# Kernel tuning notes

Measured on AMD Instinct MI355X. Metric: run time of the kernel, lower is better.

## Reference

```python
import jax, jax.numpy as jnp
import numpy as np

N_NODES = 100000
N_EDGES = 1600000
D_IN = 128
D_H = 128
N_CLASSES = 64


def setup_inputs() -> dict:
    key = jax.random.key(0)
    ks = jax.random.split(key, 8)
    feat = jax.random.normal(ks[0], (N_NODES, D_IN), dtype=jnp.float32)
    src = jax.random.randint(ks[1], (N_EDGES,), 0, N_NODES)
    dst = jax.random.randint(ks[2], (N_EDGES,), 0, N_NODES)
    # Xavier-ish scaled weights (nn.Linear layout: [out, in])
    W1 = jax.random.normal(ks[3], (D_H, D_IN), dtype=jnp.float32) * (1.0 / np.sqrt(D_IN))
    b1 = jnp.zeros((D_H,), dtype=jnp.float32)
    W2 = jax.random.normal(ks[4], (D_H, D_H), dtype=jnp.float32) * (1.0 / np.sqrt(D_H))
    b2 = jnp.zeros((D_H,), dtype=jnp.float32)
    Wl = jax.random.normal(ks[5], (N_CLASSES, 2 * D_H), dtype=jnp.float32) * (1.0 / np.sqrt(2 * D_H))
    bl = jnp.zeros((N_CLASSES,), dtype=jnp.float32)
    return {"feat": feat, "src": src, "dst": dst, "W1": W1, "b1": b1,
            "W2": W2, "b2": b2, "Wl": Wl, "bl": bl}


def _mean_agg(h, src, dst, inv_deg, n):
    # copy_u('h','m') + mean('m','neigh'): gather src features, segment-sum on dst, divide by in-degree
    s = jax.ops.segment_sum(h[src], dst, num_segments=n)  # [N, D]
    return s * inv_deg


def reference(feat, src, dst, W1, b1, W2, b2, Wl, bl):
    n = feat.shape[0]
    deg = jax.ops.segment_sum(jnp.ones_like(dst, dtype=feat.dtype), dst, num_segments=n)
    inv_deg = (1.0 / jnp.maximum(deg, 1.0))[:, None]  # zero-degree nodes -> 0 (sum is 0 anyway)
    h1 = jax.nn.relu(_mean_agg(feat, src, dst, inv_deg, n) @ W1.T + b1)
    h2 = jax.nn.relu(_mean_agg(h1, src, dst, inv_deg, n) @ W2.T + b2)
    logits = jnp.concatenate([h1, h2], axis=-1) @ Wl.T + bl
    return jax.nn.log_softmax(logits, axis=-1)
```

## Files before the change

### kernel.cpp

```cpp
#include <hip/hip_runtime.h>
#include <stdint.h>

#define D 128
#define NCLS 64
#define BSH 7
#define NBMAX 1024
#define CCHUNK 4096

typedef __bf16 bf16x8 __attribute__((ext_vector_type(8)));
typedef float f32x4 __attribute__((ext_vector_type(4)));
typedef float f32x2 __attribute__((ext_vector_type(2)));

union B8 { uint4 u; bf16x8 v; };


__global__ __launch_bounds__(256) void k_prep(const float* __restrict__ feat,
                                              const float* __restrict__ W1,
                                              const float* __restrict__ W2,
                                              const float* __restrict__ Wl,
                                              ushort* __restrict__ featb,
                                              ushort* __restrict__ W1b,
                                              ushort* __restrict__ W2b,
                                              ushort* __restrict__ Wlb,
                                              int* __restrict__ bcnt, int n8feat) {
  const int n1 = D * D / 8;
  const int nl = 2 * D * NCLS / 8;
  int t = blockIdx.x * 256 + threadIdx.x;
  if (t < NBMAX) bcnt[t] = 0;
  const float* xp; ushort* yp; int idx;
  if (t < n8feat) { xp = feat; yp = featb; idx = t; }
  else {
    t -= n8feat;
    if (t < n1) { xp = W1; yp = W1b; idx = t; }
    else if (t < 2 * n1) { xp = W2; yp = W2b; idx = t - n1; }
    else if (t < 2 * n1 + nl) { xp = Wl; yp = Wlb; idx = t - 2 * n1; }
    else return;
  }
  const float4 a = reinterpret_cast<const float4*>(xp)[idx * 2 + 0];
  const float4 b = reinterpret_cast<const float4*>(xp)[idx * 2 + 1];
  union { __bf16 h[8]; uint4 u; } p;
  p.h[0] = (__bf16)a.x; p.h[1] = (__bf16)a.y; p.h[2] = (__bf16)a.z; p.h[3] = (__bf16)a.w;
  p.h[4] = (__bf16)b.x; p.h[5] = (__bf16)b.y; p.h[6] = (__bf16)b.z; p.h[7] = (__bf16)b.w;
  reinterpret_cast<uint4*>(yp)[idx] = p.u;
}


__global__ __launch_bounds__(256) void k_bhist(const int* __restrict__ dst,
                                               int* __restrict__ bcnt, int E, int NB) {
  __shared__ int h[NBMAX];
  for (int i = threadIdx.x; i < NB; i += 256) h[i] = 0;
  __syncthreads();
  for (int e = blockIdx.x * 256 + threadIdx.x; e < E; e += gridDim.x * 256)
    atomicAdd(&h[dst[e] >> BSH], 1);
  __syncthreads();
  for (int i = threadIdx.x; i < NB; i += 256) {
    int c = h[i];
    if (c) atomicAdd(&bcnt[i], c);
  }
}

__global__ __launch_bounds__(1024) void k_bscan(const int* __restrict__ bcnt,
                                                int* __restrict__ bbase,
                                                int* __restrict__ bcur, int NB, int E) {
  __shared__ int sm[NBMAX];
  const int tid = threadIdx.x;
  int v = (tid < NB) ? bcnt[tid] : 0;
  sm[tid] = v;
  __syncthreads();
  for (int off = 1; off < NBMAX; off <<= 1) {
    int t = (tid >= off) ? sm[tid - off] : 0;
    __syncthreads();
    sm[tid] += t;
    __syncthreads();
  }
  if (tid < NB) {
    bbase[tid] = sm[tid] - v;
    bcur[tid] = sm[tid] - v;
  }
  if (tid == 0) bbase[NB] = E;
}

__global__ __launch_bounds__(256) void k_bscatter(const int* __restrict__ src,
                                                  const int* __restrict__ dst,
                                                  int* __restrict__ bcur,
                                                  int* __restrict__ ebuck, int E, int NB) {
  __shared__ int h[NBMAX];
  __shared__ int base[NBMAX];
  const int beg = blockIdx.x * CCHUNK;
  const int end = min(beg + CCHUNK, E);
  for (int i = threadIdx.x; i < NB; i += 256) h[i] = 0;
  __syncthreads();
  for (int e = beg + threadIdx.x; e < end; e += 256)
    atomicAdd(&h[dst[e] >> BSH], 1);
  __syncthreads();
  for (int i = threadIdx.x; i < NB; i += 256) {
    int c = h[i];
    base[i] = c ? atomicAdd(&bcur[i], c) : 0;
    h[i] = 0;
  }
  __syncthreads();
  for (int e = beg + threadIdx.x; e < end; e += 256) {
    const int d = dst[e];
    const int b = d >> BSH;
    const int r = atomicAdd(&h[b], 1);
    ebuck[base[b] + r] = (src[e] << BSH) | (d & 127);
  }
}

__global__ __launch_bounds__(256) void k_bbuild(const int* __restrict__ ebuck,
                                                const int* __restrict__ bbase,
                                                int* __restrict__ row_ptr,
                                                int* __restrict__ esrc,
                                                float* __restrict__ inv, int N, int E) {
  __shared__ int cnt[128], s[128], cur[128];
  const int b = blockIdx.x;
  const int n0 = b << BSH;
  const int nn = min(128, N - n0);
  const int beg = bbase[b], end = bbase[b + 1];
  const int tid = threadIdx.x;
  if (tid < 128) cnt[tid] = 0;
  __syncthreads();
  for (int e = beg + tid; e < end; e += 256)
    atomicAdd(&cnt[ebuck[e] & 127], 1);
  __syncthreads();
  if (tid < 128) s[tid] = cnt[tid];
  __syncthreads();
  for (int off = 1; off < 128; off <<= 1) {
    int t = (tid < 128 && tid >= off) ? s[tid - off] : 0;
    __syncthreads();
    if (tid < 128) s[tid] += t;
    __syncthreads();
  }
  if (tid < 128) {
    const int ex = s[tid] - cnt[tid];
    cur[tid] = ex;
    if (tid < nn) {
      row_ptr[n0 + tid] = beg + ex;
      inv[n0 + tid] = 1.0f / fmaxf((float)cnt[tid], 1.0f);
    }
  }
  if (b == 0 && tid == 0) row_ptr[N] = E;
  __syncthreads();
  for (int e = beg + tid; e < end; e += 256) {
    const int p = ebuck[e];
    const int r = atomicAdd(&cur[p & 127], 1);
    esrc[beg + r] = p >> BSH;
  }
}


__device__ __forceinline__ void accp(f32x2& a, unsigned int u) {
  f32x2 v;
  v.x = __uint_as_float(u << 16);
  v.y = __uint_as_float(u & 0xffff0000u);
  a += v;
}

__device__ __forceinline__ void acc8p(f32x2 acc[4], const uint4& u) {
  accp(acc[0], u.x);
  accp(acc[1], u.y);
  accp(acc[2], u.z);
  accp(acc[3], u.w);
}

__device__ __forceinline__ void gather_tile(const ushort* __restrict__ h,
                                            const int* __restrict__ row_ptr,
                                            const int* __restrict__ esrc,
                                            const float* __restrict__ inv,
                                            ushort At[16][136],
                                            int mt, int nl, int l15, int N) {
  const int node = mt * 16 + nl;
  const ushort* hp = h + l15 * 8;
  f32x2 acc[4] = {{0.f, 0.f}, {0.f, 0.f}, {0.f, 0.f}, {0.f, 0.f}};
  float iv = 0.f;
  if (node < N) {
    const int beg = row_ptr[node];
    const int end = row_ptr[node + 1];
    iv = inv[node];
    int e = beg;
    for (; e + 3 < end; e += 4) {
      const int4 ss = *reinterpret_cast<const int4*>(esrc + e);
      const uint4 u0 = *reinterpret_cast<const uint4*>(hp + (size_t)ss.x * D);
      const uint4 u1 = *reinterpret_cast<const uint4*>(hp + (size_t)ss.y * D);
      const uint4 u2 = *reinterpret_cast<const uint4*>(hp + (size_t)ss.z * D);
      const uint4 u3 = *reinterpret_cast<const uint4*>(hp + (size_t)ss.w * D);
      acc8p(acc, u0);
      acc8p(acc, u1);
      acc8p(acc, u2);
      acc8p(acc, u3);
    }
    for (; e < end; ++e) {
      const int s0 = esrc[e];
      const uint4 u0 = *reinterpret_cast<const uint4*>(hp + (size_t)s0 * D);
      acc8p(acc, u0);
    }
  }
  union { __bf16 b[8]; uint4 u; } p;
#pragma unroll
  for (int i = 0; i < 4; ++i) {
    p.b[i * 2 + 0] = (__bf16)(acc[i].x * iv);
    p.b[i * 2 + 1] = (__bf16)(acc[i].y * iv);
  }
  *reinterpret_cast<uint4*>(&At[nl][l15 * 8]) = p.u;
}


__global__ __launch_bounds__(256, 6) void k_fused1(const ushort* __restrict__ h,
                                                   const int* __restrict__ row_ptr,
                                                   const int* __restrict__ esrc,
                                                   const float* __restrict__ inv,
                                                   const ushort* __restrict__ Wb,
                                                   const float* __restrict__ bias,
                                                   ushort* __restrict__ Hout, int N) {
  __shared__ ushort At[16][136];
  const int wave = threadIdx.x >> 6;
  const int lane = threadIdx.x & 63;
  const int l15 = lane & 15;
  const int quad = lane >> 4;
  const int nl = wave * 4 + quad;

  B8 bfrag[2][4];
  float bv[2];
#pragma unroll
  for (int t = 0; t < 2; ++t) {
    const int n = wave * 32 + t * 16 + l15;
    bv[t] = bias[n];
#pragma unroll
    for (int ks = 0; ks < 4; ++ks)
      bfrag[t][ks].u = *reinterpret_cast<const uint4*>(Wb + n * D + ks * 32 + quad * 8);
  }

  const int mtiles = (N + 15) >> 4;
  for (int mt = blockIdx.x; mt < mtiles; mt += gridDim.x) {
    gather_tile(h, row_ptr, esrc, inv, At, mt, nl, l15, N);
    __syncthreads();
    const ushort* ap = &At[l15][quad * 8];
    B8 a0, a1, a2, a3;
    a0.u = *reinterpret_cast<const uint4*>(ap);
    a1.u = *reinterpret_cast<const uint4*>(ap + 32);
    a2.u = *reinterpret_cast<const uint4*>(ap + 64);
    a3.u = *reinterpret_cast<const uint4*>(ap + 96);
#pragma unroll
    for (int t = 0; t < 2; ++t) {
      f32x4 acc = {0.f, 0.f, 0.f, 0.f};
      acc = __builtin_amdgcn_mfma_f32_16x16x32_bf16(a0.v, bfrag[t][0].v, acc, 0, 0, 0);
      acc = __builtin_amdgcn_mfma_f32_16x16x32_bf16(a1.v, bfrag[t][1].v, acc, 0, 0, 0);
      acc = __builtin_amdgcn_mfma_f32_16x16x32_bf16(a2.v, bfrag[t][2].v, acc, 0, 0, 0);
      acc = __builtin_amdgcn_mfma_f32_16x16x32_bf16(a3.v, bfrag[t][3].v, acc, 0, 0, 0);
      const int col = wave * 32 + t * 16 + l15;
#pragma unroll
      for (int r = 0; r < 4; ++r) {
        const int row = mt * 16 + quad * 4 + r;
        if (row < N) {
          const float v = fmaxf(acc[r] + bv[t], 0.f);
          union { __bf16 b; ushort s; } c;
          c.b = (__bf16)v;
          Hout[(size_t)row * D + col] = c.s;
        }
      }
    }
    __syncthreads();
  }
}


__global__ __launch_bounds__(256, 5) void k_fused2(const ushort* __restrict__ h,
                                                   const int* __restrict__ row_ptr,
                                                   const int* __restrict__ esrc,
                                                   const float* __restrict__ inv,
                                                   const ushort* __restrict__ W2b,
                                                   const float* __restrict__ b2,
                                                   const ushort* __restrict__ Wlb,
                                                   const float* __restrict__ bl,
                                                   float* __restrict__ out, int N) {
  __shared__ ushort At[16][136];
  __shared__ ushort H2t[16][136];
  __shared__ float L[16][NCLS + 4];
  const int wave = threadIdx.x >> 6;
  const int lane = threadIdx.x & 63;
  const int l15 = lane & 15;
  const int quad = lane >> 4;
  const int nl = wave * 4 + quad;

  B8 bfrag2[2][4];
  float bv2[2];
#pragma unroll
  for (int t = 0; t < 2; ++t) {
    const int n = wave * 32 + t * 16 + l15;
    bv2[t] = b2[n];
#pragma unroll
    for (int ks = 0; ks < 4; ++ks)
      bfrag2[t][ks].u = *reinterpret_cast<const uint4*>(W2b + n * D + ks * 32 + quad * 8);
  }
  B8 bfragL[8];
  const int nlc = wave * 16 + l15;
  const float bbl = bl[nlc];
#pragma unroll
  for (int ks = 0; ks < 8; ++ks)
    bfragL[ks].u = *reinterpret_cast<const uint4*>(Wlb + nlc * (2 * D) + ks * 32 + quad * 8);

  const int mtiles = (N + 15) >> 4;
  for (int mt = blockIdx.x; mt < mtiles; mt += gridDim.x) {
    gather_tile(h, row_ptr, esrc, inv, At, mt, nl, l15, N);
    __syncthreads();
    {
      const ushort* ap = &At[l15][quad * 8];
      B8 a0, a1, a2, a3;
      a0.u = *reinterpret_cast<const uint4*>(ap);
      a1.u = *reinterpret_cast<const uint4*>(ap + 32);
      a2.u = *reinterpret_cast<const uint4*>(ap + 64);
      a3.u = *reinterpret_cast<const uint4*>(ap + 96);
#pragma unroll
      for (int t = 0; t < 2; ++t) {
        f32x4 acc = {0.f, 0.f, 0.f, 0.f};
        acc = __builtin_amdgcn_mfma_f32_16x16x32_bf16(a0.v, bfrag2[t][0].v, acc, 0, 0, 0);
        acc = __builtin_amdgcn_mfma_f32_16x16x32_bf16(a1.v, bfrag2[t][1].v, acc, 0, 0, 0);
        acc = __builtin_amdgcn_mfma_f32_16x16x32_bf16(a2.v, bfrag2[t][2].v, acc, 0, 0, 0);
        acc = __builtin_amdgcn_mfma_f32_16x16x32_bf16(a3.v, bfrag2[t][3].v, acc, 0, 0, 0);
        const int col = wave * 32 + t * 16 + l15;
#pragma unroll
        for (int r = 0; r < 4; ++r) {
          const float v = fmaxf(acc[r] + bv2[t], 0.f);
          union { __bf16 b; ushort s; } c;
          c.b = (__bf16)v;
          H2t[quad * 4 + r][col] = c.s;
        }
      }
    }
    __syncthreads();
    {
      const int row = mt * 16 + l15;
      const int rowc = row < N ? row : N - 1;
      const size_t rb = (size_t)rowc * D + quad * 8;
      f32x4 acc = {0.f, 0.f, 0.f, 0.f};
      B8 a;
#pragma unroll
      for (int ks = 0; ks < 4; ++ks) {
        a.u = *reinterpret_cast<const uint4*>(h + rb + ks * 32);
        acc = __builtin_amdgcn_mfma_f32_16x16x32_bf16(a.v, bfragL[ks].v, acc, 0, 0, 0);
      }
#pragma unroll
      for (int ks = 0; ks < 4; ++ks) {
        a.u = *reinterpret_cast<const uint4*>(&H2t[l15][ks * 32 + quad * 8]);
        acc = __builtin_amdgcn_mfma_f32_16x16x32_bf16(a.v, bfragL[4 + ks].v, acc, 0, 0, 0);
      }
#pragma unroll
      for (int r = 0; r < 4; ++r)
        L[quad * 4 + r][wave * 16 + l15] = acc[r] + bbl;
    }
    __syncthreads();
#pragma unroll
    for (int r = 0; r < 4; ++r) {
      const int row = wave * 4 + r;
      float v = L[row][lane];
      float m = v;
#pragma unroll
      for (int off = 32; off > 0; off >>= 1) m = fmaxf(m, __shfl_xor(m, off));
      float e = __expf(v - m);
#pragma unroll
      for (int off = 32; off > 0; off >>= 1) e += __shfl_xor(e, off);
      const int orow = mt * 16 + row;
      if (orow < N) out[(size_t)orow * NCLS + lane] = v - m - __logf(e);
    }
    __syncthreads();
  }
}


extern "C" void kernel_launch(void* const* d_in, const int* in_sizes, int n_in,
                              void* d_out, int out_size, void* d_ws, size_t ws_size,
                              hipStream_t stream) {
  const float* feat = (const float*)d_in[0];
  const int* src = (const int*)d_in[1];
  const int* dst = (const int*)d_in[2];
  const float* W1 = (const float*)d_in[3];
  const float* b1 = (const float*)d_in[4];
  const float* W2 = (const float*)d_in[5];
  const float* b2 = (const float*)d_in[6];
  const float* Wl = (const float*)d_in[7];
  const float* bl = (const float*)d_in[8];
  float* out = (float*)d_out;

  const int N = in_sizes[0] / D;
  const int E = in_sizes[1];
  const int NB = (N + 127) >> BSH;

  float* ws = (float*)d_ws;
  float* inv = ws;
  ushort* featb = (ushort*)(inv + N);
  ushort* scratch = featb + (size_t)N * D;
  ushort* h1b = scratch + (size_t)N * D;
  int* row_ptr = (int*)(h1b + (size_t)N * D);
  int* esrc = row_ptr + N + 1;
  int* bcnt = esrc + E;
  int* bbase = bcnt + NBMAX;
  int* bcur = bbase + NBMAX + 1;
  ushort* W1b = (ushort*)(bcur + NBMAX);
  ushort* W2b = W1b + D * D;
  ushort* Wlb = W2b + D * D;
  int* ebuck = (int*)scratch;

  const int n8 = N * D / 8;
  const int prepTot = n8 + 2 * (D * D / 8) + (2 * D * NCLS / 8);
  k_prep<<<(prepTot + 255) / 256, 256, 0, stream>>>(feat, W1, W2, Wl,
                                                    featb, W1b, W2b, Wlb, bcnt, n8);

  k_bhist<<<256, 256, 0, stream>>>(dst, bcnt, E, NB);
  k_bscan<<<1, 1024, 0, stream>>>(bcnt, bbase, bcur, NB, E);
  k_bscatter<<<(E + CCHUNK - 1) / CCHUNK, 256, 0, stream>>>(src, dst, bcur, ebuck, E, NB);
  k_bbuild<<<NB, 256, 0, stream>>>(ebuck, bbase, row_ptr, esrc, inv, N, E);

  k_fused1<<<2048, 256, 0, stream>>>(featb, row_ptr, esrc, inv, W1b, b1, h1b, N);
  k_fused2<<<2048, 256, 0, stream>>>(h1b, row_ptr, esrc, inv, W2b, b2, Wlb, bl, out, N);
}
```

Before: 391.2 us.

## Transform features before mean aggregation and drop separate bf16 prep pass

Uses linearity to apply W1 and W2 per node before the neighbor mean, so the gather kernels only sum, add bias and apply ReLU, and the dense GEMMs run as separate streaming kernels. Weights and features are converted to bf16 inside the GEMM kernels, which removes the standalone prep kernel, and the histogram counters are zeroed with a memset. The intent is a cheaper gather/GEMM split and no extra full-feature conversion pass. In exchange it adds extra launches and writes and rereads the z1/z2 intermediates, and the ebuck scratch now aliases z2.

```diff
diff --git a/kernel.cpp b/kernel.cpp
--- a/kernel.cpp
+++ b/kernel.cpp
@@ -13,35 +13,11 @@
 
 union B8 { uint4 u; bf16x8 v; };
 
-
-__global__ __launch_bounds__(256) void k_prep(const float* __restrict__ feat,
-                                              const float* __restrict__ W1,
-                                              const float* __restrict__ W2,
-                                              const float* __restrict__ Wl,
-                                              ushort* __restrict__ featb,
-                                              ushort* __restrict__ W1b,
-                                              ushort* __restrict__ W2b,
-                                              ushort* __restrict__ Wlb,
-                                              int* __restrict__ bcnt, int n8feat) {
-  const int n1 = D * D / 8;
-  const int nl = 2 * D * NCLS / 8;
-  int t = blockIdx.x * 256 + threadIdx.x;
-  if (t < NBMAX) bcnt[t] = 0;
-  const float* xp; ushort* yp; int idx;
-  if (t < n8feat) { xp = feat; yp = featb; idx = t; }
-  else {
-    t -= n8feat;
-    if (t < n1) { xp = W1; yp = W1b; idx = t; }
-    else if (t < 2 * n1) { xp = W2; yp = W2b; idx = t - n1; }
-    else if (t < 2 * n1 + nl) { xp = Wl; yp = Wlb; idx = t - 2 * n1; }
-    else return;
-  }
-  const float4 a = reinterpret_cast<const float4*>(xp)[idx * 2 + 0];
-  const float4 b = reinterpret_cast<const float4*>(xp)[idx * 2 + 1];
+__device__ __forceinline__ B8 pack8(const float4& a, const float4& b) {
   union { __bf16 h[8]; uint4 u; } p;
   p.h[0] = (__bf16)a.x; p.h[1] = (__bf16)a.y; p.h[2] = (__bf16)a.z; p.h[3] = (__bf16)a.w;
   p.h[4] = (__bf16)b.x; p.h[5] = (__bf16)b.y; p.h[6] = (__bf16)b.z; p.h[7] = (__bf16)b.w;
-  reinterpret_cast<uint4*>(yp)[idx] = p.u;
+  B8 r; r.u = p.u; return r;
 }
 
 
@@ -149,6 +125,103 @@
 }
 
 
+__global__ __launch_bounds__(256) void k_gemmz1(const float* __restrict__ A,
+                                                const float* __restrict__ W,
+                                                ushort* __restrict__ Z, int N) {
+  const int wave = threadIdx.x >> 6;
+  const int lane = threadIdx.x & 63;
+  const int l15 = lane & 15;
+  const int quad = lane >> 4;
+
+  B8 bfrag[2][4];
+#pragma unroll
+  for (int t = 0; t < 2; ++t) {
+    const int n = wave * 32 + t * 16 + l15;
+    const float* wp = W + (size_t)n * D + quad * 8;
+#pragma unroll
+    for (int ks = 0; ks < 4; ++ks)
+      bfrag[t][ks] = pack8(*reinterpret_cast<const float4*>(wp + ks * 32),
+                           *reinterpret_cast<const float4*>(wp + ks * 32 + 4));
+  }
+
+  const int mtiles = (N + 15) >> 4;
+  for (int mt = blockIdx.x; mt < mtiles; mt += gridDim.x) {
+    const int arow = min(mt * 16 + l15, N - 1);
+    const float* ap = A + (size_t)arow * D + quad * 8;
+    B8 a[4];
+#pragma unroll
+    for (int ks = 0; ks < 4; ++ks)
+      a[ks] = pack8(*reinterpret_cast<const float4*>(ap + ks * 32),
+                    *reinterpret_cast<const float4*>(ap + ks * 32 + 4));
+#pragma unroll
+    for (int t = 0; t < 2; ++t) {
+      f32x4 acc = {0.f, 0.f, 0.f, 0.f};
+#pragma unroll
+      for (int ks = 0; ks < 4; ++ks)
+        acc = __builtin_amdgcn_mfma_f32_16x16x32_bf16(a[ks].v, bfrag[t][ks].v, acc, 0, 0, 0);
+      const int col = wave * 32 + t * 16 + l15;
+#pragma unroll
+      for (int r = 0; r < 4; ++r) {
+        const int orow = mt * 16 + quad * 4 + r;
+        if (orow < N) {
+          union { __bf16 b; ushort s; } c;
+          c.b = (__bf16)acc[r];
+          Z[(size_t)orow * D + col] = c.s;
+        }
+      }
+    }
+  }
+}
+
+
+__global__ __launch_bounds__(256) void k_gemmz2(const ushort* __restrict__ A,
+                                                const float* __restrict__ W,
+                                                ushort* __restrict__ Z, int N) {
+  const int wave = threadIdx.x >> 6;
+  const int lane = threadIdx.x & 63;
+  const int l15 = lane & 15;
+  const int quad = lane >> 4;
+
+  B8 bfrag[2][4];
+#pragma unroll
+  for (int t = 0; t < 2; ++t) {
+    const int n = wave * 32 + t * 16 + l15;
+    const float* wp = W + (size_t)n * D + quad * 8;
+#pragma unroll
+    for (int ks = 0; ks < 4; ++ks)
+      bfrag[t][ks] = pack8(*reinterpret_cast<const float4*>(wp + ks * 32),
+                           *reinterpret_cast<const float4*>(wp + ks * 32 + 4));
+  }
+
+  const int mtiles = (N + 15) >> 4;
+  for (int mt = blockIdx.x; mt < mtiles; mt += gridDim.x) {
+    const int arow = min(mt * 16 + l15, N - 1);
+    const ushort* ap = A + (size_t)arow * D + quad * 8;
+    B8 a[4];
+#pragma unroll
+    for (int ks = 0; ks < 4; ++ks)
+      a[ks].u = *reinterpret_cast<const uint4*>(ap + ks * 32);
+#pragma unroll
+    for (int t = 0; t < 2; ++t) {
+      f32x4 acc = {0.f, 0.f, 0.f, 0.f};
+#pragma unroll
+      for (int ks = 0; ks < 4; ++ks)
+        acc = __builtin_amdgcn_mfma_f32_16x16x32_bf16(a[ks].v, bfrag[t][ks].v, acc, 0, 0, 0);
+      const int col = wave * 32 + t * 16 + l15;
+#pragma unroll
+      for (int r = 0; r < 4; ++r) {
+        const int orow = mt * 16 + quad * 4 + r;
+        if (orow < N) {
+          union { __bf16 b; ushort s; } c;
+          c.b = (__bf16)acc[r];
+          Z[(size_t)orow * D + col] = c.s;
+        }
+      }
+    }
+  }
+}
+
+
 __device__ __forceinline__ void accp(f32x2& a, unsigned int u) {
   f32x2 v;
   v.x = __uint_as_float(u << 16);
@@ -163,190 +236,135 @@
   accp(acc[3], u.w);
 }
 
-__device__ __forceinline__ void gather_tile(const ushort* __restrict__ h,
-                                            const int* __restrict__ row_ptr,
-                                            const int* __restrict__ esrc,
-                                            const float* __restrict__ inv,
-                                            ushort At[16][136],
-                                            int mt, int nl, int l15, int N) {
-  const int node = mt * 16 + nl;
-  const ushort* hp = h + l15 * 8;
-  f32x2 acc[4] = {{0.f, 0.f}, {0.f, 0.f}, {0.f, 0.f}, {0.f, 0.f}};
-  float iv = 0.f;
-  if (node < N) {
-    const int beg = row_ptr[node];
-    const int end = row_ptr[node + 1];
-    iv = inv[node];
-    int e = beg;
-    for (; e + 3 < end; e += 4) {
-      const int4 ss = *reinterpret_cast<const int4*>(esrc + e);
-      const uint4 u0 = *reinterpret_cast<const uint4*>(hp + (size_t)ss.x * D);
-      const uint4 u1 = *reinterpret_cast<const uint4*>(hp + (size_t)ss.y * D);
-      const uint4 u2 = *reinterpret_cast<const uint4*>(hp + (size_t)ss.z * D);
-      const uint4 u3 = *reinterpret_cast<const uint4*>(hp + (size_t)ss.w * D);
-      acc8p(acc, u0);
-      acc8p(acc, u1);
-      acc8p(acc, u2);
-      acc8p(acc, u3);
-    }
-    for (; e < end; ++e) {
-      const int s0 = esrc[e];
-      const uint4 u0 = *reinterpret_cast<const uint4*>(hp + (size_t)s0 * D);
-      acc8p(acc, u0);
-    }
-  }
-  union { __bf16 b[8]; uint4 u; } p;
-#pragma unroll
-  for (int i = 0; i < 4; ++i) {
-    p.b[i * 2 + 0] = (__bf16)(acc[i].x * iv);
-    p.b[i * 2 + 1] = (__bf16)(acc[i].y * iv);
-  }
-  *reinterpret_cast<uint4*>(&At[nl][l15 * 8]) = p.u;
-}
-
-
-__global__ __launch_bounds__(256, 6) void k_fused1(const ushort* __restrict__ h,
-                                                   const int* __restrict__ row_ptr,
-                                                   const int* __restrict__ esrc,
-                                                   const float* __restrict__ inv,
-                                                   const ushort* __restrict__ Wb,
-                                                   const float* __restrict__ bias,
-                                                   ushort* __restrict__ Hout, int N) {
-  __shared__ ushort At[16][136];
-  const int wave = threadIdx.x >> 6;
-  const int lane = threadIdx.x & 63;
-  const int l15 = lane & 15;
-  const int quad = lane >> 4;
-  const int nl = wave * 4 + quad;
-
-  B8 bfrag[2][4];
-  float bv[2];
-#pragma unroll
-  for (int t = 0; t < 2; ++t) {
-    const int n = wave * 32 + t * 16 + l15;
-    bv[t] = bias[n];
-#pragma unroll
-    for (int ks = 0; ks < 4; ++ks)
-      bfrag[t][ks].u = *reinterpret_cast<const uint4*>(Wb + n * D + ks * 32 + quad * 8);
-  }
-
-  const int mtiles = (N + 15) >> 4;
-  for (int mt = blockIdx.x; mt < mtiles; mt += gridDim.x) {
-    gather_tile(h, row_ptr, esrc, inv, At, mt, nl, l15, N);
-    __syncthreads();
-    const ushort* ap = &At[l15][quad * 8];
-    B8 a0, a1, a2, a3;
-    a0.u = *reinterpret_cast<const uint4*>(ap);
-    a1.u = *reinterpret_cast<const uint4*>(ap + 32);
-    a2.u = *reinterpret_cast<const uint4*>(ap + 64);
-    a3.u = *reinterpret_cast<const uint4*>(ap + 96);
-#pragma unroll
-    for (int t = 0; t < 2; ++t) {
-      f32x4 acc = {0.f, 0.f, 0.f, 0.f};
-      acc = __builtin_amdgcn_mfma_f32_16x16x32_bf16(a0.v, bfrag[t][0].v, acc, 0, 0, 0);
-      acc = __builtin_amdgcn_mfma_f32_16x16x32_bf16(a1.v, bfrag[t][1].v, acc, 0, 0, 0);
-      acc = __builtin_amdgcn_mfma_f32_16x16x32_bf16(a2.v, bfrag[t][2].v, acc, 0, 0, 0);
-      acc = __builtin_amdgcn_mfma_f32_16x16x32_bf16(a3.v, bfrag[t][3].v, acc, 0, 0, 0);
-      const int col = wave * 32 + t * 16 + l15;
-#pragma unroll
-      for (int r = 0; r < 4; ++r) {
-        const int row = mt * 16 + quad * 4 + r;
-        if (row < N) {
-          const float v = fmaxf(acc[r] + bv[t], 0.f);
-          union { __bf16 b; ushort s; } c;
-          c.b = (__bf16)v;
-          Hout[(size_t)row * D + col] = c.s;
-        }
-      }
-    }
-    __syncthreads();
-  }
-}
-
-
-__global__ __launch_bounds__(256, 5) void k_fused2(const ushort* __restrict__ h,
-                                                   const int* __restrict__ row_ptr,
-                                                   const int* __restrict__ esrc,
-                                                   const float* __restrict__ inv,
-                                                   const ushort* __restrict__ W2b,
-                                                   const float* __restrict__ b2,
-                                                   const ushort* __restrict__ Wlb,
-                                                   const float* __restrict__ bl,
-                                                   float* __restrict__ out, int N) {
-  __shared__ ushort At[16][136];
+__device__ __forceinline__ void gather_acc(const ushort* __restrict__ hp,
+                                           const int* __restrict__ esrc,
+                                           int beg, int end, f32x2 acc[4]) {
+  int e = beg;
+  for (; e + 3 < end; e += 4) {
+    const int4 ss = *reinterpret_cast<const int4*>(esrc + e);
+    const uint4 u0 = *reinterpret_cast<const uint4*>(hp + (size_t)ss.x * D);
+    const uint4 u1 = *reinterpret_cast<const uint4*>(hp + (size_t)ss.y * D);
+    const uint4 u2 = *reinterpret_cast<const uint4*>(hp + (size_t)ss.z * D);
+    const uint4 u3 = *reinterpret_cast<const uint4*>(hp + (size_t)ss.w * D);
+    acc8p(acc, u0);
+    acc8p(acc, u1);
+    acc8p(acc, u2);
+    acc8p(acc, u3);
+  }
+  for (; e < end; ++e) {
+    const int s0 = esrc[e];
+    const uint4 u0 = *reinterpret_cast<const uint4*>(hp + (size_t)s0 * D);
+    acc8p(acc, u0);
+  }
+}
+
+
+__global__ __launch_bounds__(256) void k_gather_relu(const ushort* __restrict__ z,
+                                                     const int* __restrict__ row_ptr,
+                                                     const int* __restrict__ esrc,
+                                                     const float* __restrict__ inv,
+                                                     const float* __restrict__ bias,
+                                                     ushort* __restrict__ out, int N) {
+  const int g = threadIdx.x >> 4;
+  const int w = threadIdx.x & 15;
+  const ushort* hp = z + w * 8;
+  float bb[8];
+  {
+    const float4 x = *reinterpret_cast<const float4*>(bias + w * 8);
+    const float4 y = *reinterpret_cast<const float4*>(bias + w * 8 + 4);
+    bb[0] = x.x; bb[1] = x.y; bb[2] = x.z; bb[3] = x.w;
+    bb[4] = y.x; bb[5] = y.y; bb[6] = y.z; bb[7] = y.w;
+  }
+  const int ntiles = (N + 15) >> 4;
+  for (int tile = blockIdx.x; tile < ntiles; tile += gridDim.x) {
+    const int node = tile * 16 + g;
+    if (node >= N) continue;
+    f32x2 acc[4] = {{0.f, 0.f}, {0.f, 0.f}, {0.f, 0.f}, {0.f, 0.f}};
+    gather_acc(hp, esrc, row_ptr[node], row_ptr[node + 1], acc);
+    const float iv = inv[node];
+    union { __bf16 b[8]; uint4 u; } p;
+#pragma unroll
+    for (int i = 0; i < 4; ++i) {
+      p.b[i * 2 + 0] = (__bf16)fmaxf(acc[i].x * iv + bb[i * 2 + 0], 0.f);
+      p.b[i * 2 + 1] = (__bf16)fmaxf(acc[i].y * iv + bb[i * 2 + 1], 0.f);
+    }
+    *reinterpret_cast<uint4*>(out + (size_t)node * D + w * 8) = p.u;
+  }
+}
+
+
+__global__ __launch_bounds__(256, 4) void k_gather_logits(const ushort* __restrict__ z2,
+                                                          const ushort* __restrict__ h1,
+                                                          const int* __restrict__ row_ptr,
+                                                          const int* __restrict__ esrc,
+                                                          const float* __restrict__ inv,
+                                                          const float* __restrict__ b2,
+                                                          const float* __restrict__ Wl,
+                                                          const float* __restrict__ bl,
+                                                          float* __restrict__ out, int N) {
   __shared__ ushort H2t[16][136];
   __shared__ float L[16][NCLS + 4];
   const int wave = threadIdx.x >> 6;
   const int lane = threadIdx.x & 63;
   const int l15 = lane & 15;
   const int quad = lane >> 4;
-  const int nl = wave * 4 + quad;
-
-  B8 bfrag2[2][4];
-  float bv2[2];
-#pragma unroll
-  for (int t = 0; t < 2; ++t) {
-    const int n = wave * 32 + t * 16 + l15;
-    bv2[t] = b2[n];
-#pragma unroll
-    for (int ks = 0; ks < 4; ++ks)
-      bfrag2[t][ks].u = *reinterpret_cast<const uint4*>(W2b + n * D + ks * 32 + quad * 8);
+  const int g = threadIdx.x >> 4;
+  const int w = threadIdx.x & 15;
+  const ushort* hp = z2 + w * 8;
+
+  float bb[8];
+  {
+    const float4 x = *reinterpret_cast<const float4*>(b2 + w * 8);
+    const float4 y = *reinterpret_cast<const float4*>(b2 + w * 8 + 4);
+    bb[0] = x.x; bb[1] = x.y; bb[2] = x.z; bb[3] = x.w;
+    bb[4] = y.x; bb[5] = y.y; bb[6] = y.z; bb[7] = y.w;
   }
   B8 bfragL[8];
   const int nlc = wave * 16 + l15;
   const float bbl = bl[nlc];
-#pragma unroll
-  for (int ks = 0; ks < 8; ++ks)
-    bfragL[ks].u = *reinterpret_cast<const uint4*>(Wlb + nlc * (2 * D) + ks * 32 + quad * 8);
+  {
+    const float* wp = Wl + (size_t)nlc * (2 * D) + quad * 8;
+#pragma unroll
+    for (int ks = 0; ks < 8; ++ks)
+      bfragL[ks] = pack8(*reinterpret_cast<const float4*>(wp + ks * 32),
+                         *reinterpret_cast<const float4*>(wp + ks * 32 + 4));
+  }
 
   const int mtiles = (N + 15) >> 4;
   for (int mt = blockIdx.x; mt < mtiles; mt += gridDim.x) {
-    gather_tile(h, row_ptr, esrc, inv, At, mt, nl, l15, N);
+    const int node = mt * 16 + g;
+    f32x2 acc[4] = {{0.f, 0.f}, {0.f, 0.f}, {0.f, 0.f}, {0.f, 0.f}};
+    float iv = 0.f;
+    if (node < N) {
+      gather_acc(hp, esrc, row_ptr[node], row_ptr[node + 1], acc);
+      iv = inv[node];
+    }
+    union { __bf16 b[8]; uint4 u; } p;
+#pragma unroll
+    for (int i = 0; i < 4; ++i) {
+      p.b[i * 2 + 0] = (__bf16)fmaxf(acc[i].x * iv + bb[i * 2 + 0], 0.f);
+      p.b[i * 2 + 1] = (__bf16)fmaxf(acc[i].y * iv + bb[i * 2 + 1], 0.f);
+    }
+    *reinterpret_cast<uint4*>(&H2t[g][w * 8]) = p.u;
     __syncthreads();
     {
-      const ushort* ap = &At[l15][quad * 8];
-      B8 a0, a1, a2, a3;
-      a0.u = *reinterpret_cast<const uint4*>(ap);
-      a1.u = *reinterpret_cast<const uint4*>(ap + 32);
-      a2.u = *reinterpret_cast<const uint4*>(ap + 64);
-      a3.u = *reinterpret_cast<const uint4*>(ap + 96);
-#pragma unroll
-      for (int t = 0; t < 2; ++t) {
-        f32x4 acc = {0.f, 0.f, 0.f, 0.f};
-        acc = __builtin_amdgcn_mfma_f32_16x16x32_bf16(a0.v, bfrag2[t][0].v, acc, 0, 0, 0);
-        acc = __builtin_amdgcn_mfma_f32_16x16x32_bf16(a1.v, bfrag2[t][1].v, acc, 0, 0, 0);
-        acc = __builtin_amdgcn_mfma_f32_16x16x32_bf16(a2.v, bfrag2[t][2].v, acc, 0, 0, 0);
-        acc = __builtin_amdgcn_mfma_f32_16x16x32_bf16(a3.v, bfrag2[t][3].v, acc, 0, 0, 0);
-        const int col = wave * 32 + t * 16 + l15;
-#pragma unroll
-        for (int r = 0; r < 4; ++r) {
-          const float v = fmaxf(acc[r] + bv2[t], 0.f);
-          union { __bf16 b; ushort s; } c;
-          c.b = (__bf16)v;
-          H2t[quad * 4 + r][col] = c.s;
-        }
-      }
-    }
-    __syncthreads();
-    {
-      const int row = mt * 16 + l15;
-      const int rowc = row < N ? row : N - 1;
-      const size_t rb = (size_t)rowc * D + quad * 8;
-      f32x4 acc = {0.f, 0.f, 0.f, 0.f};
+      const int arow = min(mt * 16 + l15, N - 1);
+      const ushort* h1p = h1 + (size_t)arow * D + quad * 8;
+      f32x4 acL = {0.f, 0.f, 0.f, 0.f};
       B8 a;
 #pragma unroll
       for (int ks = 0; ks < 4; ++ks) {
-        a.u = *reinterpret_cast<const uint4*>(h + rb + ks * 32);
-        acc = __builtin_amdgcn_mfma_f32_16x16x32_bf16(a.v, bfragL[ks].v, acc, 0, 0, 0);
+        a.u = *reinterpret_cast<const uint4*>(h1p + ks * 32);
+        acL = __builtin_amdgcn_mfma_f32_16x16x32_bf16(a.v, bfragL[ks].v, acL, 0, 0, 0);
       }
 #pragma unroll
       for (int ks = 0; ks < 4; ++ks) {
         a.u = *reinterpret_cast<const uint4*>(&H2t[l15][ks * 32 + quad * 8]);
-        acc = __builtin_amdgcn_mfma_f32_16x16x32_bf16(a.v, bfragL[4 + ks].v, acc, 0, 0, 0);
+        acL = __builtin_amdgcn_mfma_f32_16x16x32_bf16(a.v, bfragL[4 + ks].v, acL, 0, 0, 0);
       }
 #pragma unroll
       for (int r = 0; r < 4; ++r)
-        L[quad * 4 + r][wave * 16 + l15] = acc[r] + bbl;
+        L[quad * 4 + r][wave * 16 + l15] = acL[r] + bbl;
     }
     __syncthreads();
 #pragma unroll
@@ -387,29 +405,25 @@
 
   float* ws = (float*)d_ws;
   float* inv = ws;
-  ushort* featb = (ushort*)(inv + N);
-  ushort* scratch = featb + (size_t)N * D;
-  ushort* h1b = scratch + (size_t)N * D;
-  int* row_ptr = (int*)(h1b + (size_t)N * D);
+  ushort* z1 = (ushort*)(inv + N);
+  ushort* h1b = z1 + (size_t)N * D;
+  ushort* z2 = h1b + (size_t)N * D;
+  int* row_ptr = (int*)(z2 + (size_t)N * D);
   int* esrc = row_ptr + N + 1;
   int* bcnt = esrc + E;
   int* bbase = bcnt + NBMAX;
   int* bcur = bbase + NBMAX + 1;
-  ushort* W1b = (ushort*)(bcur + NBMAX);
-  ushort* W2b = W1b + D * D;
-  ushort* Wlb = W2b + D * D;
-  int* ebuck = (int*)scratch;
-
-  const int n8 = N * D / 8;
-  const int prepTot = n8 + 2 * (D * D / 8) + (2 * D * NCLS / 8);
-  k_prep<<<(prepTot + 255) / 256, 256, 0, stream>>>(feat, W1, W2, Wl,
-                                                    featb, W1b, W2b, Wlb, bcnt, n8);
-
+  int* ebuck = (int*)z2;
+
+  hipMemsetAsync(bcnt, 0, NBMAX * sizeof(int), stream);
   k_bhist<<<256, 256, 0, stream>>>(dst, bcnt, E, NB);
   k_bscan<<<1, 1024, 0, stream>>>(bcnt, bbase, bcur, NB, E);
   k_bscatter<<<(E + CCHUNK - 1) / CCHUNK, 256, 0, stream>>>(src, dst, bcur, ebuck, E, NB);
   k_bbuild<<<NB, 256, 0, stream>>>(ebuck, bbase, row_ptr, esrc, inv, N, E);
 
-  k_fused1<<<2048, 256, 0, stream>>>(featb, row_ptr, esrc, inv, W1b, b1, h1b, N);
-  k_fused2<<<2048, 256, 0, stream>>>(h1b, row_ptr, esrc, inv, W2b, b2, Wlb, bl, out, N);
-}
+  k_gemmz1<<<2048, 256, 0, stream>>>(feat, W1, z1, N);
+  k_gather_relu<<<2048, 256, 0, stream>>>(z1, row_ptr, esrc, inv, b1, h1b, N);
+
+  k_gemmz2<<<2048, 256, 0, stream>>>(h1b, W2, z2, N);
+  k_gather_logits<<<2048, 256, 0, stream>>>(z2, h1b, row_ptr, esrc, inv, b2, Wl, bl, out, N);
+}
```

Result: slower. 401.3 us (+2.6%).
